# Performance work log

Measured on AMD Instinct MI355X. Metric: run time of the kernel, lower is better.

The kernel has to match this reference:

```python
import jax, jax.numpy as jnp
import numpy as np


def setup_inputs() -> dict:
    key = jax.random.key(0)
    ks = jax.random.split(key, 6)
    N, Tx, Ty = 8, 1024, 128
    enc_dim, dec_dim, Ca = 512, 1024, 128
    sc = 0.02
    return {
        "h": jax.random.normal(ks[0], (N, Tx, enc_dim), jnp.float32),
        "s": jax.random.normal(ks[1], (N, Ty, dec_dim), jnp.float32),
        "Wh": jax.random.normal(ks[2], (enc_dim, Ca), jnp.float32) * sc,
        "Ws": jax.random.normal(ks[3], (dec_dim, Ca), jnp.float32) * sc,
        "b": jax.random.normal(ks[4], (Ca,), jnp.float32) * sc,
        "v": jax.random.normal(ks[5], (Ca,), jnp.float32) * sc,
    }


def reference(h, s, Wh, Ws, b, v):
    # W([h;s]) + b == h@Wh + s@Ws + b (split of the concat Linear weight)
    ph = jnp.einsum("nxc,ca->nxa", h, Wh)            # (N, Tx, Ca)
    ps = jnp.einsum("nyd,da->nya", s, Ws) + b        # (N, Ty, Ca)
    # broadcast-add -> tanh -> dot with v : (N, Ty, Tx)
    e = jnp.einsum("nyxa,a->nyx", jnp.tanh(ps[:, :, None, :] + ph[:, None, :, :]), v)
    return jax.nn.softmax(e, axis=-1)                # attention over Tx
```

## Files before the change

### kernel.cpp

```cpp
#include <hip/hip_runtime.h>
#include <stdint.h>


typedef float  f32x4  __attribute__((ext_vector_type(4)));
typedef float  f32x2  __attribute__((ext_vector_type(2)));
typedef __bf16 bf16x8 __attribute__((ext_vector_type(8)));

#define LOG2E     1.4426950408889634f
#define TWO_LOG2E 2.8853900817779268f

static __device__ __forceinline__ f32x2 sp2(float s) {
    return (f32x2){s, s};
}

__global__ void __launch_bounds__(256) transpose_cast(
    const float* __restrict__ Wh, const float* __restrict__ Ws,
    __bf16* __restrict__ WhT, __bf16* __restrict__ WsT)
{
    int bid = blockIdx.x;
    const float* src; __bf16* dst; int K, c0;
    if (bid < 32) { src = Wh; dst = WhT; K = 512;  c0 = bid * 16; }
    else          { src = Ws; dst = WsT; K = 1024; c0 = (bid - 32) * 16; }
    __shared__ float tile[16][129];
    int t = threadIdx.x;
    #pragma unroll
    for (int i = 0; i < 2048; i += 256) {
        int idx = i + t;
        int r = idx >> 7, col = idx & 127;
        tile[r][col] = src[(size_t)(c0 + r) * 128 + col];
    }
    __syncthreads();
    #pragma unroll
    for (int i = 0; i < 2048; i += 256) {
        int idx = i + t;
        int a = idx >> 4, cc = idx & 15;
        dst[(size_t)a * K + c0 + cc] = (__bf16)tile[cc][a];
    }
}

__global__ void __launch_bounds__(256) gemm_fused(
    const __bf16* __restrict__ WhT, const __bf16* __restrict__ WsT,
    const float* __restrict__ h, const float* __restrict__ s,
    float* __restrict__ Eph, float* __restrict__ psPart)
{
    int bid = blockIdx.x;
    int tid = threadIdx.x, lane = tid & 63, w = tid >> 6;
    int mq = w * 32;
    int q = lane >> 4, c = lane & 15;

    const __bf16* A; const float* B; float* Cp; int K, kbase, colg; bool isPs;
    if (bid < 512) {
        isPs = false; A = WhT; B = h; K = 512; kbase = 0;
        colg = bid * 16;
        int n = colg >> 10, x = colg & 1023;
        Cp = Eph + (size_t)n * 131072 + x;
    } else {
        isPs = true; A = WsT; B = s; K = 1024;
        int b2 = bid - 512;
        int half = b2 & 1; kbase = half * 512;
        colg = (b2 >> 1) * 16;
        Cp = psPart + (size_t)half * 131072 + colg;
    }

    const float*  Bp = B + (size_t)(colg + c) * K + kbase + q * 8;
    const __bf16* Ap = A + (size_t)(mq + c) * K + kbase + q * 8;

    f32x4 acc0 = {}, acc1 = {};
    float4 b0s[4], b1s[4];
    bf16x8 a0s[4], a1s[4];
    #pragma unroll
    for (int p = 0; p < 4; ++p) {
        int k = p * 32;
        b0s[p] = *(const float4*)(Bp + k);
        b1s[p] = *(const float4*)(Bp + k + 4);
        a0s[p] = *(const bf16x8*)(Ap + k);
        a1s[p] = *(const bf16x8*)(Ap + (size_t)16 * K + k);
    }
    #pragma unroll
    for (int it = 0; it < 16; ++it) {
        int cur = it & 3;
        float4 b0 = b0s[cur], b1 = b1s[cur];
        bf16x8 bf;
        bf[0] = (__bf16)b0.x; bf[1] = (__bf16)b0.y;
        bf[2] = (__bf16)b0.z; bf[3] = (__bf16)b0.w;
        bf[4] = (__bf16)b1.x; bf[5] = (__bf16)b1.y;
        bf[6] = (__bf16)b1.z; bf[7] = (__bf16)b1.w;
        acc0 = __builtin_amdgcn_mfma_f32_16x16x32_bf16(a0s[cur], bf, acc0, 0, 0, 0);
        acc1 = __builtin_amdgcn_mfma_f32_16x16x32_bf16(a1s[cur], bf, acc1, 0, 0, 0);
        if (it + 4 < 16) {
            int k = (it + 4) * 32;
            b0s[cur] = *(const float4*)(Bp + k);
            b1s[cur] = *(const float4*)(Bp + k + 4);
            a0s[cur] = *(const bf16x8*)(Ap + k);
            a1s[cur] = *(const bf16x8*)(Ap + (size_t)16 * K + k);
        }
    }

    #pragma unroll
    for (int i = 0; i < 2; ++i) {
        f32x4 av = i ? acc1 : acc0;
        #pragma unroll
        for (int r = 0; r < 4; ++r) {
            int m = mq + i * 16 + q * 4 + r;
            if (isPs) Cp[(size_t)m * 1024 + c] = av[r];
            else      Cp[(size_t)m * 1024 + c] =
                          __builtin_amdgcn_exp2f(av[r] * TWO_LOG2E);
        }
    }
}

__global__ void __launch_bounds__(512) attn_softmax(
    const float* __restrict__ Eph, const float* __restrict__ psPart,
    const float* __restrict__ bias, const float* __restrict__ v,
    float* __restrict__ out)
{
    int bid = blockIdx.x;
    int n = bid & 7, yg = bid >> 3;
    int ny = n * 128 + yg * 4;
    const f32x2* ph2 = (const f32x2*)(Eph + (size_t)n * 131072);
    int t = threadIdx.x;

    __shared__ f32x4 eps4[128];
    __shared__ f32x4 vv4[32];
    __shared__ float wred[4][8];
    __shared__ float VsumS;

    if (t < 128) {
        f32x4 pa = *(const f32x4*)(psPart + (size_t)t * 1024 + ny);
        f32x4 pb = *(const f32x4*)(psPart + 131072 + (size_t)t * 1024 + ny);
        float bb = bias[t];
        f32x4 pk;
        #pragma unroll
        for (int j = 0; j < 4; ++j)
            pk[j] = __builtin_amdgcn_exp2f((pa[j] + pb[j] + bb) * TWO_LOG2E);
        eps4[t] = pk;
    } else if (t < 160) {
        vv4[t - 128] = *(const f32x4*)(v + (t - 128) * 4);
    }
    if (t >= 448) {
        int l = t - 448;
        float vv = v[l] + v[l + 64];
        for (int m = 32; m; m >>= 1) vv += __shfl_xor(vv, m);
        if (l == 0) VsumS = vv;
    }
    __syncthreads();
    float Vsum = VsumS;

    f32x2 accv[4] = {};
    f32x2 p[4]; f32x4 q[4]; f32x4 vr;
    #pragma unroll
    for (int i = 0; i < 4; ++i) p[i] = ph2[i * 512 + t];
    #pragma unroll
    for (int i = 0; i < 4; ++i) q[i] = eps4[i];
    vr = vv4[0];

    #pragma unroll 2
    for (int a = 0; a < 128; a += 4) {
        int an = (a + 4 < 128) ? a + 4 : a;
        f32x2 np[4]; f32x4 nq[4];
        #pragma unroll
        for (int i = 0; i < 4; ++i) np[i] = ph2[(an + i) * 512 + t];
        #pragma unroll
        for (int i = 0; i < 4; ++i) nq[i] = eps4[an + i];
        f32x4 nvr = vv4[an >> 2];

        f32x2 v0 = sp2(vr[0]), v1 = sp2(vr[1]);
        f32x2 v2 = sp2(vr[2]), v3 = sp2(vr[3]);
        f32x2 one = sp2(1.f);
        #pragma unroll
        for (int j = 0; j < 4; ++j) {
            f32x2 w0 = __builtin_elementwise_fma(sp2(q[0][j]), p[0], one);
            f32x2 w1 = __builtin_elementwise_fma(sp2(q[1][j]), p[1], one);
            f32x2 w2 = __builtin_elementwise_fma(sp2(q[2][j]), p[2], one);
            f32x2 w3 = __builtin_elementwise_fma(sp2(q[3][j]), p[3], one);
            f32x2 d01 = w0 * w1, d23 = w2 * w3;
            f32x2 n01 = __builtin_elementwise_fma(v1, w0, v0 * w1);
            f32x2 n23 = __builtin_elementwise_fma(v3, w2, v2 * w3);
            f32x2 dd = d01 * d23;
            f32x2 nn = __builtin_elementwise_fma(n23, d01, n01 * d23);
            f32x2 r;
            r.x = __builtin_amdgcn_rcpf(dd.x);
            r.y = __builtin_amdgcn_rcpf(dd.y);
            accv[j] = __builtin_elementwise_fma(nn, r, accv[j]);
        }
        #pragma unroll
        for (int i = 0; i < 4; ++i) { p[i] = np[i]; q[i] = nq[i]; }
        vr = nvr;
    }

    float e[4][2];
    #pragma unroll
    for (int j = 0; j < 4; ++j) {
        e[j][0] = fmaf(-2.f, accv[j].x, Vsum);
        e[j][1] = fmaf(-2.f, accv[j].y, Vsum);
    }

    int lane = t & 63, wv = t >> 6;
    float mx[4];
    #pragma unroll
    for (int j = 0; j < 4; ++j) {
        mx[j] = fmaxf(e[j][0], e[j][1]);
        for (int m = 32; m; m >>= 1) mx[j] = fmaxf(mx[j], __shfl_xor(mx[j], m));
    }
    if (lane == 0) {
        #pragma unroll
        for (int j = 0; j < 4; ++j) wred[j][wv] = mx[j];
    }
    __syncthreads();
    #pragma unroll
    for (int j = 0; j < 4; ++j) {
        mx[j] = wred[j][0];
        #pragma unroll
        for (int i = 1; i < 8; ++i) mx[j] = fmaxf(mx[j], wred[j][i]);
    }
    __syncthreads();
    float sx[4][2], sm[4];
    #pragma unroll
    for (int j = 0; j < 4; ++j) {
        sx[j][0] = __builtin_amdgcn_exp2f((e[j][0] - mx[j]) * LOG2E);
        sx[j][1] = __builtin_amdgcn_exp2f((e[j][1] - mx[j]) * LOG2E);
        sm[j] = sx[j][0] + sx[j][1];
        for (int m = 32; m; m >>= 1) sm[j] += __shfl_xor(sm[j], m);
    }
    if (lane == 0) {
        #pragma unroll
        for (int j = 0; j < 4; ++j) wred[j][wv] = sm[j];
    }
    __syncthreads();
    #pragma unroll
    for (int j = 0; j < 4; ++j) {
        float smj = 0.f;
        #pragma unroll
        for (int i = 0; i < 8; ++i) smj += wred[j][i];
        float r = __builtin_amdgcn_rcpf(smj);
        float2 o; o.x = sx[j][0] * r; o.y = sx[j][1] * r;
        ((float2*)(out + (size_t)(ny + j) * 1024))[t] = o;
    }
}

extern "C" void kernel_launch(void* const* d_in, const int* in_sizes, int n_in,
                              void* d_out, int out_size, void* d_ws, size_t ws_size,
                              hipStream_t stream) {
    const float* h  = (const float*)d_in[0];
    const float* s  = (const float*)d_in[1];
    const float* Wh = (const float*)d_in[2];
    const float* Ws = (const float*)d_in[3];
    const float* b  = (const float*)d_in[4];
    const float* v  = (const float*)d_in[5];
    float* out = (float*)d_out;

    char* ws = (char*)d_ws;
    float*  Eph    = (float*)ws;
    float*  psPart = (float*)(ws + (4u << 20));
    __bf16* WhT    = (__bf16*)(ws + (5u << 20));
    __bf16* WsT    = WhT + (size_t)128 * 512;

    transpose_cast<<<96, 256, 0, stream>>>(Wh, Ws, WhT, WsT);
    gemm_fused<<<640, 256, 0, stream>>>(WhT, WsT, h, s, Eph, psPart);
    attn_softmax<<<256, 512, 0, stream>>>(Eph, psPart, b, v, out);
}
```

Baseline: 111.8 us.

## Combine eight tanh terms per reciprocal and interleave GEMM blocks across batches

```diff
diff --git a/kernel.cpp b/kernel.cpp
--- a/kernel.cpp
+++ b/kernel.cpp
@@ -51,14 +51,15 @@
     const __bf16* A; const float* B; float* Cp; int K, kbase, colg; bool isPs;
     if (bid < 512) {
         isPs = false; A = WhT; B = h; K = 512; kbase = 0;
-        colg = bid * 16;
-        int n = colg >> 10, x = colg & 1023;
-        Cp = Eph + (size_t)n * 131072 + x;
+        int n = bid & 7, xg = bid >> 3;
+        colg = n * 1024 + xg * 16;
+        Cp = Eph + (size_t)n * 131072 + xg * 16;
     } else {
         isPs = true; A = WsT; B = s; K = 1024;
         int b2 = bid - 512;
-        int half = b2 & 1; kbase = half * 512;
-        colg = (b2 >> 1) * 16;
+        int n = b2 & 7, idx = b2 >> 3;
+        int half = idx & 1; kbase = half * 512;
+        colg = n * 128 + (idx >> 1) * 16;
         Cp = psPart + (size_t)half * 131072 + colg;
     }
 
@@ -147,25 +148,25 @@
     float Vsum = VsumS;
 
     f32x2 accv[4] = {};
-    f32x2 p[4]; f32x4 q[4]; f32x4 vr;
-    #pragma unroll
-    for (int i = 0; i < 4; ++i) p[i] = ph2[i * 512 + t];
-    #pragma unroll
-    for (int i = 0; i < 4; ++i) q[i] = eps4[i];
-    vr = vv4[0];
-
-    #pragma unroll 2
-    for (int a = 0; a < 128; a += 4) {
-        int an = (a + 4 < 128) ? a + 4 : a;
-        f32x2 np[4]; f32x4 nq[4];
-        #pragma unroll
-        for (int i = 0; i < 4; ++i) np[i] = ph2[(an + i) * 512 + t];
-        #pragma unroll
-        for (int i = 0; i < 4; ++i) nq[i] = eps4[an + i];
-        f32x4 nvr = vv4[an >> 2];
-
-        f32x2 v0 = sp2(vr[0]), v1 = sp2(vr[1]);
-        f32x2 v2 = sp2(vr[2]), v3 = sp2(vr[3]);
+    f32x2 p[8]; f32x4 q[8]; f32x4 vrA, vrB;
+    #pragma unroll
+    for (int i = 0; i < 8; ++i) p[i] = ph2[i * 512 + t];
+    #pragma unroll
+    for (int i = 0; i < 8; ++i) q[i] = eps4[i];
+    vrA = vv4[0]; vrB = vv4[1];
+
+    for (int a = 0; a < 128; a += 8) {
+        int an = (a + 8 < 128) ? a + 8 : a;
+        f32x2 np[8]; f32x4 nq[8];
+        #pragma unroll
+        for (int i = 0; i < 8; ++i) np[i] = ph2[(an + i) * 512 + t];
+        #pragma unroll
+        for (int i = 0; i < 8; ++i) nq[i] = eps4[an + i];
+        f32x4 nvrA = vv4[an >> 2], nvrB = vv4[(an >> 2) + 1];
+
+        f32x2 vvp[8];
+        #pragma unroll
+        for (int i = 0; i < 4; ++i) { vvp[i] = sp2(vrA[i]); vvp[4 + i] = sp2(vrB[i]); }
         f32x2 one = sp2(1.f);
         #pragma unroll
         for (int j = 0; j < 4; ++j) {
@@ -173,19 +174,28 @@
             f32x2 w1 = __builtin_elementwise_fma(sp2(q[1][j]), p[1], one);
             f32x2 w2 = __builtin_elementwise_fma(sp2(q[2][j]), p[2], one);
             f32x2 w3 = __builtin_elementwise_fma(sp2(q[3][j]), p[3], one);
-            f32x2 d01 = w0 * w1, d23 = w2 * w3;
-            f32x2 n01 = __builtin_elementwise_fma(v1, w0, v0 * w1);
-            f32x2 n23 = __builtin_elementwise_fma(v3, w2, v2 * w3);
-            f32x2 dd = d01 * d23;
-            f32x2 nn = __builtin_elementwise_fma(n23, d01, n01 * d23);
+            f32x2 w4 = __builtin_elementwise_fma(sp2(q[4][j]), p[4], one);
+            f32x2 w5 = __builtin_elementwise_fma(sp2(q[5][j]), p[5], one);
+            f32x2 w6 = __builtin_elementwise_fma(sp2(q[6][j]), p[6], one);
+            f32x2 w7 = __builtin_elementwise_fma(sp2(q[7][j]), p[7], one);
+            f32x2 d01 = w0 * w1, d23 = w2 * w3, d45 = w4 * w5, d67 = w6 * w7;
+            f32x2 n01 = __builtin_elementwise_fma(vvp[1], w0, vvp[0] * w1);
+            f32x2 n23 = __builtin_elementwise_fma(vvp[3], w2, vvp[2] * w3);
+            f32x2 n45 = __builtin_elementwise_fma(vvp[5], w4, vvp[4] * w5);
+            f32x2 n67 = __builtin_elementwise_fma(vvp[7], w6, vvp[6] * w7);
+            f32x2 dA = d01 * d23, dB = d45 * d67;
+            f32x2 nA = __builtin_elementwise_fma(n23, d01, n01 * d23);
+            f32x2 nB = __builtin_elementwise_fma(n67, d45, n45 * d67);
+            f32x2 dd = dA * dB;
+            f32x2 nn = __builtin_elementwise_fma(nB, dA, nA * dB);
             f32x2 r;
             r.x = __builtin_amdgcn_rcpf(dd.x);
             r.y = __builtin_amdgcn_rcpf(dd.y);
             accv[j] = __builtin_elementwise_fma(nn, r, accv[j]);
         }
         #pragma unroll
-        for (int i = 0; i < 4; ++i) { p[i] = np[i]; q[i] = nq[i]; }
-        vr = nvr;
+        for (int i = 0; i < 8; ++i) { p[i] = np[i]; q[i] = nq[i]; }
+        vrA = nvrA; vrB = nvrB;
     }
 
     float e[4][2];
```

Measured after the change: 117.4 us. +5.0%, slower.
